# Kernel optimization log

Measured on AMD Instinct MI355X. Metric: run time of the kernel, lower is better.

Reference implementation:

```python
import jax, jax.numpy as jnp
import numpy as np

B, S, D = 4, 2048, 1024
DQ = DK = DV = 1024

def setup_inputs() -> dict:
    key = jax.random.key(0)
    ks = jax.random.split(key, 7)
    s = 1.0 / np.sqrt(D)
    return {
        "X": jax.random.normal(ks[0], (B, S, D), dtype=jnp.float32),
        "Wq": jax.random.normal(ks[1], (D, DQ), dtype=jnp.float32) * s,
        "bq": jax.random.normal(ks[2], (DQ,), dtype=jnp.float32) * 0.01,
        "Wk": jax.random.normal(ks[3], (D, DK), dtype=jnp.float32) * s,
        "bk": jax.random.normal(ks[4], (DK,), dtype=jnp.float32) * 0.01,
        "Wv": jax.random.normal(ks[5], (D, DV), dtype=jnp.float32) * s,
        "bv": jax.random.normal(ks[6], (DV,), dtype=jnp.float32) * 0.01,
    }

def reference(X, Wq, bq, Wk, bk, Wv, bv):
    q = jnp.einsum('bsd,de->bse', X, Wq) + bq  # [B,S,DQ]
    k = jnp.einsum('bsd,de->bse', X, Wk) + bk  # [B,S,DK]
    v = jnp.einsum('bsd,de->bse', X, Wv) + bv  # [B,S,DV]
    scores = jnp.einsum('bqe,bke->bqk', q, k) / jnp.sqrt(jnp.float32(DK))
    attn = jax.nn.softmax(scores, axis=-1)
    return jnp.einsum('bqk,bkv->bqv', attn, v)
```

## Files before the change

kernel.cpp:

```cpp
#include <hip/hip_runtime.h>

typedef __bf16 bf16;
typedef __attribute__((ext_vector_type(8))) __bf16 bf16x8;
typedef __attribute__((ext_vector_type(4))) __bf16 bf16x4;
typedef __attribute__((ext_vector_type(4))) float f32x4;

typedef __attribute__((address_space(1))) const void GvPtr;
typedef __attribute__((address_space(3))) void LdsPtr;

__device__ __forceinline__ void gload_lds16(const void* g, void* l) {
    __builtin_amdgcn_global_load_lds((GvPtr*)g, (LdsPtr*)l, 16, 0, 0);
}

__global__ __launch_bounds__(256) void prep(
    const void* __restrict__ X,
    const void* __restrict__ Wq, const void* __restrict__ Wk,
    const void* __restrict__ Wv,
    const void* __restrict__ bq, const void* __restrict__ bk,
    const void* __restrict__ bv,
    bf16* __restrict__ Xb, bf16* __restrict__ wt, bf16* __restrict__ bb)
{
    __shared__ int sflag;
    __shared__ bf16 t[32][33];
    const int tid = threadIdx.x;

    if (tid < 64) {
        const unsigned short* H = (const unsigned short*)X;
        int insane = 0;
        for (int i = tid; i < 128; i += 64) {
            int e = (H[2 * i] >> 7) & 0xFF;
            insane += (e >= 107 && e <= 131) ? 0 : 1;
        }
        #pragma unroll
        for (int off = 32; off > 0; off >>= 1)
            insane += __shfl_down(insane, off, 64);
        if (tid == 0) sflag = (insane >= 32) ? 1 : 0;
    }
    __syncthreads();
    const bool isf32 = (sflag != 0);

    const long b = blockIdx.x;
    if (b < 4096) {
        long i = b * 256 + tid;
        if (isf32) {
            const float4* s = (const float4*)X;
            float4 a = s[2 * i], c = s[2 * i + 1];
            bf16x8 o;
            o[0] = (bf16)a.x; o[1] = (bf16)a.y; o[2] = (bf16)a.z; o[3] = (bf16)a.w;
            o[4] = (bf16)c.x; o[5] = (bf16)c.y; o[6] = (bf16)c.z; o[7] = (bf16)c.w;
            ((bf16x8*)Xb)[i] = o;
        } else {
            ((uint4*)Xb)[i] = ((const uint4*)X)[i];
        }
    } else if (b < 7168) {
        const int wi = (int)((b - 4096) >> 10);
        const int id = (int)((b - 4096) & 1023);
        const void* src = (wi == 0) ? Wq : (wi == 1) ? Wk : Wv;
        bf16* dst = wt + (long)wi * 1024 * 1024;
        const int c0 = (id & 31) * 32, r0 = (id >> 5) * 32;
        const int tc = tid & 31, tr = tid >> 5;
        #pragma unroll
        for (int i = 0; i < 4; i++) {
            long idx = (long)(r0 + tr + i * 8) * 1024 + c0 + tc;
            t[tr + i * 8][tc] = isf32 ? (bf16)((const float*)src)[idx]
                                      : ((const bf16*)src)[idx];
        }
        __syncthreads();
        #pragma unroll
        for (int i = 0; i < 4; i++)
            dst[(long)(c0 + tr + i * 8) * 1024 + r0 + tc] = t[tc][tr + i * 8];
    } else {
        const int bi = (int)(b - 7168);
        const int wi = bi >> 2;
        const void* src = (wi == 0) ? bq : (wi == 1) ? bk : bv;
        const long i = (bi & 3) * 256 + tid;
        bb[wi * 1024 + i] = isf32 ? (bf16)((const float*)src)[i]
                                  : ((const bf16*)src)[i];
    }
}

template <bool HAS_BIAS, bool OUT_F32, int WAVES, bool VSPLIT>
__global__ __launch_bounds__(WAVES * 64, 4) void gemm_bt(
    const bf16* __restrict__ A, const bf16* __restrict__ B,
    void* __restrict__ Cv, const bf16* __restrict__ bias,
    bf16* __restrict__ vt,
    int K, long lda, long ldb, long ldc, float scale,
    long strideA, long strideB, long strideC)
{
    constexpr int BK = 64;
    constexpr int MI = (WAVES == 4) ? 4 : 2;
    constexpr int NCH = (WAVES == 4) ? 4 : 2;
    constexpr int RSTEP = WAVES * 8;
    constexpr int LSTEP = WAVES * 64 * 8;

    __shared__ bf16 As[128 * BK];
    __shared__ bf16 Bs[128 * BK];

    const int tid  = threadIdx.x;
    const int wave = tid >> 6;
    const int lane = tid & 63;
    const int r16  = lane & 15;
    const int quad = lane >> 4;

    const long z = blockIdx.z;
    A += z * strideA;
    B += z * strideB;

    const int tX = gridDim.x;
    const int pid = blockIdx.y * tX + blockIdx.x;
    const int groupSize = 8 * tX;
    const int gid = pid / groupSize;
    const int rem = pid % groupSize;
    const int tileM = (gid * 8 + (rem & 7)) * 128;
    const int tileN = (rem >> 3) * 128;

    const int waveM = (wave >> 1) * ((WAVES == 4) ? 64 : 32);
    const int waveN = (wave & 1) * 64;

    const int rS = tid >> 3;
    const int cOff = (((tid & 7) - (tid >> 3)) & 7) * 8;
    const bf16* Ag[NCH]; const bf16* Bg[NCH];
    #pragma unroll
    for (int j = 0; j < NCH; j++) {
        Ag[j] = A + (long)(tileM + rS + j * RSTEP) * lda + cOff;
        Bg[j] = B + (long)(tileN + rS + j * RSTEP) * ldb + cOff;
    }

    f32x4 acc[MI][4] = {};

    for (int k0 = 0; k0 < K; k0 += BK) {
        #pragma unroll
        for (int j = 0; j < NCH; j++) {
            gload_lds16(Ag[j], &As[tid * 8 + j * LSTEP]);
            gload_lds16(Bg[j], &Bs[tid * 8 + j * LSTEP]);
            Ag[j] += BK; Bg[j] += BK;
        }
        __syncthreads();

        #pragma unroll
        for (int ks = 0; ks < 2; ks++) {
            bf16x8 af[MI], bfv[4];
            #pragma unroll
            for (int i = 0; i < MI; i++) {
                const int row = waveM + i * 16 + r16;
                af[i] = *(const bf16x8*)
                    &As[row * 64 + ((ks * 4 + quad + row) & 7) * 8];
            }
            #pragma unroll
            for (int i = 0; i < 4; i++) {
                const int row = waveN + i * 16 + r16;
                bfv[i] = *(const bf16x8*)
                    &Bs[row * 64 + ((ks * 4 + quad + row) & 7) * 8];
            }
            #pragma unroll
            for (int mi = 0; mi < MI; mi++)
                #pragma unroll
                for (int ni = 0; ni < 4; ni++)
                    acc[mi][ni] = __builtin_amdgcn_mfma_f32_16x16x32_bf16(
                        af[mi], bfv[ni], acc[mi][ni], 0, 0, 0);
        }
        __syncthreads();
    }

    const int crow0 = tileM + waveM + quad * 4;
    const int ccol0 = tileN + waveN + r16;

    if (VSPLIT && tileN >= 2048) {
        #pragma unroll
        for (int ni = 0; ni < 4; ni++) {
            const int col = ccol0 + ni * 16;
            const float bv = HAS_BIAS ? (float)bias[col] : 0.0f;
            const long colp = col - 2048;
            #pragma unroll
            for (int mi = 0; mi < MI; mi++) {
                const int grow = crow0 + mi * 16;
                const long bz = grow >> 11;
                const int srow = grow & 2047;
                bf16x4 o;
                #pragma unroll
                for (int r = 0; r < 4; r++)
                    o[r] = (bf16)(acc[mi][ni][r] * scale + bv);
                *(bf16x4*)&vt[(bz << 21) + colp * 2048 + srow] = o;
            }
        }
    } else {
        #pragma unroll
        for (int ni = 0; ni < 4; ni++) {
            const int col = ccol0 + ni * 16;
            const float bv = HAS_BIAS ? (float)bias[col] : 0.0f;
            #pragma unroll
            for (int mi = 0; mi < MI; mi++) {
                #pragma unroll
                for (int r = 0; r < 4; r++) {
                    const long row = crow0 + mi * 16 + r;
                    const float val = acc[mi][ni][r] * scale + bv;
                    if (OUT_F32) ((float*)Cv)[z * strideC + row * ldc + col] = val;
                    else         ((bf16*)Cv)[z * strideC + row * ldc + col] = (bf16)val;
                }
            }
        }
    }
}

__global__ __launch_bounds__(256) void softmax_rows(
    const bf16* __restrict__ S, bf16* __restrict__ P)
{
    const long row = blockIdx.x;
    const bf16x8* s = (const bf16x8*)(S + row * 2048);
    const int tid = threadIdx.x;

    bf16x8 a = s[tid];
    float v[8];
    float mx = -1e30f;
    #pragma unroll
    for (int i = 0; i < 8; i++) { v[i] = (float)a[i]; mx = fmaxf(mx, v[i]); }
    #pragma unroll
    for (int off = 32; off > 0; off >>= 1)
        mx = fmaxf(mx, __shfl_down(mx, off, 64));
    __shared__ float redm[4];
    if ((tid & 63) == 0) redm[tid >> 6] = mx;
    __syncthreads();
    mx = fmaxf(fmaxf(redm[0], redm[1]), fmaxf(redm[2], redm[3]));

    float sum = 0.0f;
    #pragma unroll
    for (int i = 0; i < 8; i++) { v[i] = __expf(v[i] - mx); sum += v[i]; }
    #pragma unroll
    for (int off = 32; off > 0; off >>= 1)
        sum += __shfl_down(sum, off, 64);
    __shared__ float reds[4];
    if ((tid & 63) == 0) reds[tid >> 6] = sum;
    __syncthreads();
    const float inv = 1.0f / (reds[0] + reds[1] + reds[2] + reds[3]);

    bf16x8 o;
    #pragma unroll
    for (int i = 0; i < 8; i++) o[i] = (bf16)(v[i] * inv);
    ((bf16x8*)(P + row * 2048))[tid] = o;
}

extern "C" void kernel_launch(void* const* d_in, const int* in_sizes, int n_in,
                              void* d_out, int out_size, void* d_ws, size_t ws_size,
                              hipStream_t stream) {
    constexpr int B = 4, S = 2048, D = 1024, N = 1024;
    constexpr long MS = (long)B * S;

    const void* X  = d_in[0];
    const void* Wq = d_in[1];
    const void* bq = d_in[2];
    const void* Wk = d_in[3];
    const void* bk = d_in[4];
    const void* Wv = d_in[5];
    const void* bv = d_in[6];

    char* w = (char*)d_ws;
    bf16* Xb  = (bf16*)w;                w += MS * D * sizeof(bf16);
    bf16* wt  = (bf16*)w;                w += 3L * D * N * sizeof(bf16);
    bf16* bb  = (bf16*)w;                w += 3L * N * sizeof(bf16) + 512;
    bf16* qkv = (bf16*)w;                w += MS * 3L * N * sizeof(bf16);
    bf16* vt  = (bf16*)w;                w += MS * N * sizeof(bf16);
    bf16* sc  = (bf16*)w;                w += (long)B * S * S * sizeof(bf16);
    bf16* pr  = (bf16*)w;

    bf16* q = qkv;
    bf16* k = qkv + N;

    prep<<<7180, 256, 0, stream>>>(X, Wq, Wk, Wv, bq, bk, bv, Xb, wt, bb);

    gemm_bt<true, false, 4, true><<<dim3(3 * N / 128, MS / 128, 1), 256, 0, stream>>>(
        Xb, wt, qkv, bb, vt, D, D, D, 3L * N, 1.0f, 0, 0, 0);

    gemm_bt<false, false, 4, false><<<dim3(S / 128, S / 128, B), 256, 0, stream>>>(
        q, k, sc, nullptr, nullptr, D, 3L * N, 3L * N, S, 0.03125f,
        (long)S * 3 * N, (long)S * 3 * N, (long)S * S);

    softmax_rows<<<B * S, 256, 0, stream>>>(sc, pr);

    gemm_bt<false, true, 8, false><<<dim3(N / 128, S / 128, B), 512, 0, stream>>>(
        pr, vt, d_out, nullptr, nullptr, S, S, S, N, 1.0f,
        (long)S * S, (long)N * S, (long)S * N);
}
```

Measured before the change: 254.8 us.

## Fuse softmax into QK^T epilogue and defer normalization to PV GEMM

The separate softmax kernel is removed. The QK^T GEMM epilogue now writes exp(scaled score) as bf16 and accumulates per-row sums with wave shuffles plus float atomics into a zeroed buffer. A new dedicated PV GEMM with BK=128 and 4 waves divides its output by the row sum in its epilogue. This cuts one full read/write pass over the B*S*S score matrix and a kernel launch. The cost is dropping max subtraction, which risks overflow for large scores, plus atomic traffic and a memset.

```diff
diff --git a/kernel.cpp b/kernel.cpp
--- a/kernel.cpp
+++ b/kernel.cpp
@@ -79,20 +79,15 @@
     }
 }
 
-template <bool HAS_BIAS, bool OUT_F32, int WAVES, bool VSPLIT>
-__global__ __launch_bounds__(WAVES * 64, 4) void gemm_bt(
+template <bool HAS_BIAS, bool OUT_F32, bool VSPLIT, bool EXPSUM>
+__global__ __launch_bounds__(256, 4) void gemm_bt(
     const bf16* __restrict__ A, const bf16* __restrict__ B,
     void* __restrict__ Cv, const bf16* __restrict__ bias,
-    bf16* __restrict__ vt,
+    bf16* __restrict__ vt, float* __restrict__ rowsum,
     int K, long lda, long ldb, long ldc, float scale,
     long strideA, long strideB, long strideC)
 {
     constexpr int BK = 64;
-    constexpr int MI = (WAVES == 4) ? 4 : 2;
-    constexpr int NCH = (WAVES == 4) ? 4 : 2;
-    constexpr int RSTEP = WAVES * 8;
-    constexpr int LSTEP = WAVES * 64 * 8;
-
     __shared__ bf16 As[128 * BK];
     __shared__ bf16 Bs[128 * BK];
 
@@ -114,34 +109,34 @@
     const int tileM = (gid * 8 + (rem & 7)) * 128;
     const int tileN = (rem >> 3) * 128;
 
-    const int waveM = (wave >> 1) * ((WAVES == 4) ? 64 : 32);
+    const int waveM = (wave >> 1) * 64;
     const int waveN = (wave & 1) * 64;
 
     const int rS = tid >> 3;
     const int cOff = (((tid & 7) - (tid >> 3)) & 7) * 8;
-    const bf16* Ag[NCH]; const bf16* Bg[NCH];
+    const bf16* Ag[4]; const bf16* Bg[4];
     #pragma unroll
-    for (int j = 0; j < NCH; j++) {
-        Ag[j] = A + (long)(tileM + rS + j * RSTEP) * lda + cOff;
-        Bg[j] = B + (long)(tileN + rS + j * RSTEP) * ldb + cOff;
-    }
-
-    f32x4 acc[MI][4] = {};
+    for (int j = 0; j < 4; j++) {
+        Ag[j] = A + (long)(tileM + rS + j * 32) * lda + cOff;
+        Bg[j] = B + (long)(tileN + rS + j * 32) * ldb + cOff;
+    }
+
+    f32x4 acc[4][4] = {};
 
     for (int k0 = 0; k0 < K; k0 += BK) {
         #pragma unroll
-        for (int j = 0; j < NCH; j++) {
-            gload_lds16(Ag[j], &As[tid * 8 + j * LSTEP]);
-            gload_lds16(Bg[j], &Bs[tid * 8 + j * LSTEP]);
+        for (int j = 0; j < 4; j++) {
+            gload_lds16(Ag[j], &As[tid * 8 + j * 2048]);
+            gload_lds16(Bg[j], &Bs[tid * 8 + j * 2048]);
             Ag[j] += BK; Bg[j] += BK;
         }
         __syncthreads();
 
         #pragma unroll
         for (int ks = 0; ks < 2; ks++) {
-            bf16x8 af[MI], bfv[4];
-            #pragma unroll
-            for (int i = 0; i < MI; i++) {
+            bf16x8 af[4], bfv[4];
+            #pragma unroll
+            for (int i = 0; i < 4; i++) {
                 const int row = waveM + i * 16 + r16;
                 af[i] = *(const bf16x8*)
                     &As[row * 64 + ((ks * 4 + quad + row) & 7) * 8];
@@ -153,7 +148,7 @@
                     &Bs[row * 64 + ((ks * 4 + quad + row) & 7) * 8];
             }
             #pragma unroll
-            for (int mi = 0; mi < MI; mi++)
+            for (int mi = 0; mi < 4; mi++)
                 #pragma unroll
                 for (int ni = 0; ni < 4; ni++)
                     acc[mi][ni] = __builtin_amdgcn_mfma_f32_16x16x32_bf16(
@@ -165,14 +160,47 @@
     const int crow0 = tileM + waveM + quad * 4;
     const int ccol0 = tileN + waveN + r16;
 
-    if (VSPLIT && tileN >= 2048) {
+    if (EXPSUM) {
+        float rs[4][4];
+        #pragma unroll
+        for (int mi = 0; mi < 4; mi++)
+            #pragma unroll
+            for (int r = 0; r < 4; r++) rs[mi][r] = 0.0f;
+        #pragma unroll
+        for (int ni = 0; ni < 4; ni++) {
+            const int col = ccol0 + ni * 16;
+            #pragma unroll
+            for (int mi = 0; mi < 4; mi++) {
+                #pragma unroll
+                for (int r = 0; r < 4; r++) {
+                    const long row = crow0 + mi * 16 + r;
+                    const float p = __expf(acc[mi][ni][r] * scale);
+                    rs[mi][r] += p;
+                    ((bf16*)Cv)[z * strideC + row * ldc + col] = (bf16)p;
+                }
+            }
+        }
+        #pragma unroll
+        for (int mi = 0; mi < 4; mi++) {
+            #pragma unroll
+            for (int r = 0; r < 4; r++) {
+                float s = rs[mi][r];
+                s += __shfl_xor(s, 1, 64);
+                s += __shfl_xor(s, 2, 64);
+                s += __shfl_xor(s, 4, 64);
+                s += __shfl_xor(s, 8, 64);
+                if (r16 == 0)
+                    atomicAdd(&rowsum[z * 2048 + crow0 + mi * 16 + r], s);
+            }
+        }
+    } else if (VSPLIT && tileN >= 2048) {
         #pragma unroll
         for (int ni = 0; ni < 4; ni++) {
             const int col = ccol0 + ni * 16;
             const float bv = HAS_BIAS ? (float)bias[col] : 0.0f;
             const long colp = col - 2048;
             #pragma unroll
-            for (int mi = 0; mi < MI; mi++) {
+            for (int mi = 0; mi < 4; mi++) {
                 const int grow = crow0 + mi * 16;
                 const long bz = grow >> 11;
                 const int srow = grow & 2047;
@@ -189,7 +217,7 @@
             const int col = ccol0 + ni * 16;
             const float bv = HAS_BIAS ? (float)bias[col] : 0.0f;
             #pragma unroll
-            for (int mi = 0; mi < MI; mi++) {
+            for (int mi = 0; mi < 4; mi++) {
                 #pragma unroll
                 for (int r = 0; r < 4; r++) {
                     const long row = crow0 + mi * 16 + r;
@@ -202,41 +230,97 @@
     }
 }
 
-__global__ __launch_bounds__(256) void softmax_rows(
-    const bf16* __restrict__ S, bf16* __restrict__ P)
+__global__ __launch_bounds__(256, 2) void gemm_pv(
+    const bf16* __restrict__ A, const bf16* __restrict__ B,
+    float* __restrict__ C, const float* __restrict__ rowsum,
+    int K, long lda, long ldb, long ldc,
+    long strideA, long strideB, long strideC)
 {
-    const long row = blockIdx.x;
-    const bf16x8* s = (const bf16x8*)(S + row * 2048);
-    const int tid = threadIdx.x;
-
-    bf16x8 a = s[tid];
-    float v[8];
-    float mx = -1e30f;
+    constexpr int BK = 128;
+    __shared__ bf16 As[128 * BK];
+    __shared__ bf16 Bs[128 * BK];
+
+    const int tid  = threadIdx.x;
+    const int wave = tid >> 6;
+    const int lane = tid & 63;
+    const int r16  = lane & 15;
+    const int quad = lane >> 4;
+
+    const long z = blockIdx.z;
+    A += z * strideA;
+    B += z * strideB;
+
+    const int tX = gridDim.x;
+    const int pid = blockIdx.y * tX + blockIdx.x;
+    const int groupSize = 8 * tX;
+    const int gid = pid / groupSize;
+    const int rem = pid % groupSize;
+    const int tileM = (gid * 8 + (rem & 7)) * 128;
+    const int tileN = (rem >> 3) * 128;
+
+    const int waveM = (wave >> 1) * 64;
+    const int waveN = (wave & 1) * 64;
+
+    const int rS = tid >> 4;
+    const int cOff = (((tid & 15) - (tid >> 4)) & 15) * 8;
+    const bf16* Ag = A + (long)(tileM + rS) * lda + cOff;
+    const bf16* Bg = B + (long)(tileN + rS) * ldb + cOff;
+
+    f32x4 acc[4][4] = {};
+
+    for (int k0 = 0; k0 < K; k0 += BK) {
+        #pragma unroll
+        for (int j = 0; j < 8; j++) {
+            gload_lds16(Ag + (long)j * 16 * lda, &As[(tid + j * 256) * 8]);
+            gload_lds16(Bg + (long)j * 16 * ldb, &Bs[(tid + j * 256) * 8]);
+        }
+        Ag += BK; Bg += BK;
+        __syncthreads();
+
+        #pragma unroll
+        for (int ks = 0; ks < 4; ks++) {
+            bf16x8 af[4], bfv[4];
+            #pragma unroll
+            for (int i = 0; i < 4; i++) {
+                const int row = waveM + i * 16 + r16;
+                af[i] = *(const bf16x8*)
+                    &As[row * 128 + ((ks * 4 + quad + row) & 15) * 8];
+            }
+            #pragma unroll
+            for (int i = 0; i < 4; i++) {
+                const int row = waveN + i * 16 + r16;
+                bfv[i] = *(const bf16x8*)
+                    &Bs[row * 128 + ((ks * 4 + quad + row) & 15) * 8];
+            }
+            #pragma unroll
+            for (int mi = 0; mi < 4; mi++)
+                #pragma unroll
+                for (int ni = 0; ni < 4; ni++)
+                    acc[mi][ni] = __builtin_amdgcn_mfma_f32_16x16x32_bf16(
+                        af[mi], bfv[ni], acc[mi][ni], 0, 0, 0);
+        }
+        __syncthreads();
+    }
+
+    const int crow0 = tileM + waveM + quad * 4;
+    const int ccol0 = tileN + waveN + r16;
+    float inv[4][4];
     #pragma unroll
-    for (int i = 0; i < 8; i++) { v[i] = (float)a[i]; mx = fmaxf(mx, v[i]); }
+    for (int mi = 0; mi < 4; mi++)
+        #pragma unroll
+        for (int r = 0; r < 4; r++)
+            inv[mi][r] = 1.0f / rowsum[z * 2048 + crow0 + mi * 16 + r];
     #pragma unroll
-    for (int off = 32; off > 0; off >>= 1)
-        mx = fmaxf(mx, __shfl_down(mx, off, 64));
-    __shared__ float redm[4];
-    if ((tid & 63) == 0) redm[tid >> 6] = mx;
-    __syncthreads();
-    mx = fmaxf(fmaxf(redm[0], redm[1]), fmaxf(redm[2], redm[3]));
-
-    float sum = 0.0f;
-    #pragma unroll
-    for (int i = 0; i < 8; i++) { v[i] = __expf(v[i] - mx); sum += v[i]; }
-    #pragma unroll
-    for (int off = 32; off > 0; off >>= 1)
-        sum += __shfl_down(sum, off, 64);
-    __shared__ float reds[4];
-    if ((tid & 63) == 0) reds[tid >> 6] = sum;
-    __syncthreads();
-    const float inv = 1.0f / (reds[0] + reds[1] + reds[2] + reds[3]);
-
-    bf16x8 o;
-    #pragma unroll
-    for (int i = 0; i < 8; i++) o[i] = (bf16)(v[i] * inv);
-    ((bf16x8*)(P + row * 2048))[tid] = o;
+    for (int ni = 0; ni < 4; ni++) {
+        const int col = ccol0 + ni * 16;
+        #pragma unroll
+        for (int mi = 0; mi < 4; mi++)
+            #pragma unroll
+            for (int r = 0; r < 4; r++) {
+                const long row = crow0 + mi * 16 + r;
+                C[z * strideC + row * ldc + col] = acc[mi][ni][r] * inv[mi][r];
+            }
+    }
 }
 
 extern "C" void kernel_launch(void* const* d_in, const int* in_sizes, int n_in,
@@ -254,29 +338,29 @@
     const void* bv = d_in[6];
 
     char* w = (char*)d_ws;
-    bf16* Xb  = (bf16*)w;                w += MS * D * sizeof(bf16);
-    bf16* wt  = (bf16*)w;                w += 3L * D * N * sizeof(bf16);
-    bf16* bb  = (bf16*)w;                w += 3L * N * sizeof(bf16) + 512;
-    bf16* qkv = (bf16*)w;                w += MS * 3L * N * sizeof(bf16);
-    bf16* vt  = (bf16*)w;                w += MS * N * sizeof(bf16);
-    bf16* sc  = (bf16*)w;                w += (long)B * S * S * sizeof(bf16);
-    bf16* pr  = (bf16*)w;
+    bf16*  Xb = (bf16*)w;                w += MS * D * sizeof(bf16);
+    bf16*  wt = (bf16*)w;                w += 3L * D * N * sizeof(bf16);
+    bf16*  bb = (bf16*)w;                w += 3L * N * sizeof(bf16) + 512;
+    float* rowsum = (float*)w;           w += MS * sizeof(float);
+    bf16*  qkv = (bf16*)w;               w += MS * 3L * N * sizeof(bf16);
+    bf16*  vt = (bf16*)w;                w += MS * N * sizeof(bf16);
+    bf16*  sc = (bf16*)w;
 
     bf16* q = qkv;
     bf16* k = qkv + N;
 
+    hipMemsetAsync(rowsum, 0, MS * sizeof(float), stream);
+
     prep<<<7180, 256, 0, stream>>>(X, Wq, Wk, Wv, bq, bk, bv, Xb, wt, bb);
 
-    gemm_bt<true, false, 4, true><<<dim3(3 * N / 128, MS / 128, 1), 256, 0, stream>>>(
-        Xb, wt, qkv, bb, vt, D, D, D, 3L * N, 1.0f, 0, 0, 0);
-
-    gemm_bt<false, false, 4, false><<<dim3(S / 128, S / 128, B), 256, 0, stream>>>(
-        q, k, sc, nullptr, nullptr, D, 3L * N, 3L * N, S, 0.03125f,
+    gemm_bt<true, false, true, false><<<dim3(3 * N / 128, MS / 128, 1), 256, 0, stream>>>(
+        Xb, wt, qkv, bb, vt, nullptr, D, D, D, 3L * N, 1.0f, 0, 0, 0);
+
+    gemm_bt<false, false, false, true><<<dim3(S / 128, S / 128, B), 256, 0, stream>>>(
+        q, k, sc, nullptr, nullptr, rowsum, D, 3L * N, 3L * N, S, 0.03125f,
         (long)S * 3 * N, (long)S * 3 * N, (long)S * S);
 
-    softmax_rows<<<B * S, 256, 0, stream>>>(sc, pr);
-
-    gemm_bt<false, true, 8, false><<<dim3(N / 128, S / 128, B), 512, 0, stream>>>(
-        pr, vt, d_out, nullptr, nullptr, S, S, S, N, 1.0f,
+    gemm_pv<<<dim3(N / 128, S / 128, B), 256, 0, stream>>>(
+        sc, vt, (float*)d_out, rowsum, S, S, S, N,
         (long)S * S, (long)N * S, (long)S * N);
 }
```

Result: no change. 250.0 us (-1.9%).
